# Kernel tuning notes

Hardware: AMD Instinct MI355X
Metric: run time of the kernel (lower is better)

The kernel has to match this reference:

```python
import jax, jax.numpy as jnp
import numpy as np

DIM = 512
DIM_EDGES = 64
LN_EPS = 1e-5


def setup_inputs() -> dict:
    key = jax.random.key(0)
    ks = jax.random.split(key, 4)
    b, n = 2, 768
    x = jax.random.normal(ks[0], (b, n, DIM), dtype=jnp.float32)
    # nn.Linear weights stored as [out, in], applied as x @ W.T
    W_rows = jax.random.normal(ks[1], (DIM_EDGES, DIM), dtype=jnp.float32) / np.sqrt(DIM)
    W_cols = jax.random.normal(ks[2], (DIM_EDGES, DIM), dtype=jnp.float32) / np.sqrt(DIM)
    W_edges = jax.random.normal(ks[3], (DIM_EDGES, DIM_EDGES), dtype=jnp.float32) / np.sqrt(DIM_EDGES)
    ln_gamma = jnp.ones((DIM_EDGES,), dtype=jnp.float32)
    ln_beta = jnp.zeros((DIM_EDGES,), dtype=jnp.float32)
    return {"x": x, "W_rows": W_rows, "W_cols": W_cols, "W_edges": W_edges,
            "ln_gamma": ln_gamma, "ln_beta": ln_beta}


def reference(x, W_rows, W_cols, W_edges, ln_gamma, ln_beta):
    # rows/cols: [b, n, d_e]
    rows = jnp.einsum('bnd,ed->bne', x, W_rows)
    cols = jnp.einsum('bnd,ed->bne', x, W_cols)
    # outer sum: [b, i, j, d_e]
    outer = rows[:, :, None, :] + cols[:, None, :, :]
    # edge linear (no bias): [b, i, j, d_e]
    h = jnp.einsum('bije,fe->bijf', outer, W_edges)
    # LayerNorm over last dim
    mu = jnp.mean(h, axis=-1, keepdims=True)
    var = jnp.mean(jnp.square(h - mu), axis=-1, keepdims=True)
    out = (h - mu) * jax.lax.rsqrt(var + LN_EPS) * ln_gamma + ln_beta
    return out
```

## Files before the change

### kernel.cpp

```cpp
#include <hip/hip_runtime.h>

#define B 2
#define N 768
#define DIM 512
#define DE 64
#define LN_EPS 1e-5f

#define OFF_RC   0
#define OFF_CC   (B*N*DE)
#define OFF_SSR  (2*B*N*DE)
#define OFF_SSC  (2*B*N*DE + B*N)

__global__ __launch_bounds__(256) void ee_precompute(
    const float* __restrict__ x, const float* __restrict__ Wr,
    const float* __restrict__ Wc, const float* __restrict__ We,
    float* __restrict__ Rc, float* __restrict__ Cc,
    float* __restrict__ ssqR, float* __restrict__ ssqC)
{
    __shared__ float xs[DIM];
    __shared__ float rc[2 * DE];

    const int tok = blockIdx.x;
    const int tid = threadIdx.x;
    const int lane = tid & 63;
    const int wave = tid >> 6;

    const float* xp = x + (size_t)tok * DIM;
    xs[tid]       = xp[tid];
    xs[tid + 256] = xp[tid + 256];
    __syncthreads();

    const float4 b0 = *(const float4*)(xs + lane * 8);
    const float4 b1 = *(const float4*)(xs + lane * 8 + 4);
    for (int m = 0; m < 32; ++m) {
        const int o = wave * 32 + m;
        const float* W = (o < DE) ? (Wr + (size_t)o * DIM)
                                  : (Wc + (size_t)(o - DE) * DIM);
        const float4 a0 = *(const float4*)(W + lane * 8);
        const float4 a1 = *(const float4*)(W + lane * 8 + 4);
        float p = a0.x*b0.x + a0.y*b0.y + a0.z*b0.z + a0.w*b0.w
                + a1.x*b1.x + a1.y*b1.y + a1.z*b1.z + a1.w*b1.w;
        #pragma unroll
        for (int s = 1; s < 64; s <<= 1) p += __shfl_xor(p, s);
        if (lane == 0) rc[o] = p;
    }
    __syncthreads();

    if (tid < 128) {
        const int f = lane;
        const float* W = We + (size_t)f * DE;
        const float* rcp = (wave == 0) ? rc : (rc + DE);
        float acc = 0.f;
        #pragma unroll
        for (int e4 = 0; e4 < DE / 4; ++e4) {
            const float4 w4 = *(const float4*)(W + e4 * 4);
            const float4 r4 = *(const float4*)(rcp + e4 * 4);
            acc += w4.x*r4.x + w4.y*r4.y + w4.z*r4.z + w4.w*r4.w;
        }
        float mu = acc;
        #pragma unroll
        for (int s = 1; s < 64; s <<= 1) mu += __shfl_xor(mu, s);
        mu *= (1.f / DE);
        const float c = acc - mu;
        float sq = c * c;
        #pragma unroll
        for (int s = 1; s < 64; s <<= 1) sq += __shfl_xor(sq, s);
        float* dst = ((wave == 0) ? Rc : Cc) + (size_t)tok * DE;
        dst[f] = c;
        if (lane == 0) ((wave == 0) ? ssqR : ssqC)[tok] = sq;
    }
}

__global__ __launch_bounds__(256) void ee_outer_ln(
    const float* __restrict__ Rc, const float* __restrict__ Cc,
    const float* __restrict__ ssqRp, const float* __restrict__ ssqCp,
    const float* __restrict__ gamma, const float* __restrict__ beta,
    float* __restrict__ out)
{
    const int bi = blockIdx.x;
    const int tid = threadIdx.x;
    const int lane = tid & 63;
    const int wave = tid >> 6;
    const int jsub = lane >> 4;
    const int fb = (lane & 15) * 4;

    const int b = bi / N;
    const float* Ccb   = Cc + (size_t)b * N * DE;
    const float* ssqCb = ssqCp + (size_t)b * N;
    float* outb = out + (size_t)bi * N * DE;

    const float ssqR = ssqRp[bi];
    const float4 r  = *(const float4*)(Rc + (size_t)bi * DE + fb);
    const float4 g  = *(const float4*)(gamma + fb);
    const float4 be = *(const float4*)(beta + fb);

    for (int t = 0; t < N / 16; ++t) {
        const int j = t * 16 + wave * 4 + jsub;
        const float4 c = *(const float4*)(Ccb + (size_t)j * DE + fb);
        const float ssqC = ssqCb[j];

        float p = r.x*c.x + r.y*c.y + r.z*c.z + r.w*c.w;
        p += __shfl_xor(p, 1);
        p += __shfl_xor(p, 2);
        p += __shfl_xor(p, 4);
        p += __shfl_xor(p, 8);

        const float var = (ssqR + ssqC + 2.f * p) * (1.f / DE);
        const float s = rsqrtf(var + LN_EPS);

        float4 o;
        o.x = (r.x + c.x) * (s * g.x) + be.x;
        o.y = (r.y + c.y) * (s * g.y) + be.y;
        o.z = (r.z + c.z) * (s * g.z) + be.z;
        o.w = (r.w + c.w) * (s * g.w) + be.w;
        *(float4*)(outb + (size_t)j * DE + fb) = o;
    }
}

extern "C" void kernel_launch(void* const* d_in, const int* in_sizes, int n_in,
                              void* d_out, int out_size, void* d_ws, size_t ws_size,
                              hipStream_t stream) {
    const float* x     = (const float*)d_in[0];
    const float* Wr    = (const float*)d_in[1];
    const float* Wc    = (const float*)d_in[2];
    const float* We    = (const float*)d_in[3];
    const float* gamma = (const float*)d_in[4];
    const float* beta  = (const float*)d_in[5];
    float* out = (float*)d_out;
    float* ws  = (float*)d_ws;

    float* Rc   = ws + OFF_RC;
    float* Cc   = ws + OFF_CC;
    float* ssqR = ws + OFF_SSR;
    float* ssqC = ws + OFF_SSC;

    ee_precompute<<<B * N, 256, 0, stream>>>(x, Wr, Wc, We, Rc, Cc, ssqR, ssqC);
    ee_outer_ln<<<B * N, 256, 0, stream>>>(Rc, Cc, ssqR, ssqC, gamma, beta, out);
}
```

Baseline: 343.5 us.

## Precompute per-column LN scales in LDS and use nontemporal output stores

The outer-LN kernel now runs a first pass in which each thread computes the full 64-wide dot product between the row vector (staged in LDS) and one column vector, then stores the rsqrt scale for all 768 columns in shared memory. This removes the per-iteration cross-lane shuffle reduction from the main store loop. The main loop is unrolled by four, and its 256MB output write uses nontemporal stores to avoid polluting the cache. The trade-off is a second read of the Cc matrix per block and a block-wide barrier. The strided per-thread row reads in the first pass may also be uncoalesced.

New measurement: 357.6 us. 1.04x slower.

```diff
diff --git a/kernel.cpp b/kernel.cpp
--- a/kernel.cpp
+++ b/kernel.cpp
@@ -5,6 +5,8 @@
 #define DIM 512
 #define DE 64
 #define LN_EPS 1e-5f
+
+typedef float f32x4 __attribute__((ext_vector_type(4)));
 
 #define OFF_RC   0
 #define OFF_CC   (B*N*DE)
@@ -77,6 +79,9 @@
     const float* __restrict__ gamma, const float* __restrict__ beta,
     float* __restrict__ out)
 {
+    __shared__ float rs[DE];
+    __shared__ float sj[N];
+
     const int bi = blockIdx.x;
     const int tid = threadIdx.x;
     const int lane = tid & 63;
@@ -89,31 +94,39 @@
     const float* ssqCb = ssqCp + (size_t)b * N;
     float* outb = out + (size_t)bi * N * DE;
 
+    if (tid < DE) rs[tid] = Rc[(size_t)bi * DE + tid];
+    __syncthreads();
+
     const float ssqR = ssqRp[bi];
-    const float4 r  = *(const float4*)(Rc + (size_t)bi * DE + fb);
-    const float4 g  = *(const float4*)(gamma + fb);
-    const float4 be = *(const float4*)(beta + fb);
 
+    #pragma unroll
+    for (int jt = 0; jt < N / 256; ++jt) {
+        const int j0 = jt * 256 + tid;
+        const float* cj = Ccb + (size_t)j0 * DE;
+        f32x4 a = (f32x4)(0.f);
+        #pragma unroll
+        for (int e = 0; e < DE / 4; ++e) {
+            const f32x4 w = *(const f32x4*)(rs + e * 4);
+            const f32x4 c = *(const f32x4*)(cj + e * 4);
+            a += w * c;
+        }
+        const float p = a.x + a.y + a.z + a.w;
+        const float var = (ssqR + ssqCb[j0] + 2.f * p) * (1.f / DE);
+        sj[j0] = rsqrtf(var + LN_EPS);
+    }
+    __syncthreads();
+
+    const f32x4 r  = *(const f32x4*)(rs + fb);
+    const f32x4 g  = *(const f32x4*)(gamma + fb);
+    const f32x4 be = *(const f32x4*)(beta + fb);
+
+    #pragma unroll 4
     for (int t = 0; t < N / 16; ++t) {
         const int j = t * 16 + wave * 4 + jsub;
-        const float4 c = *(const float4*)(Ccb + (size_t)j * DE + fb);
-        const float ssqC = ssqCb[j];
-
-        float p = r.x*c.x + r.y*c.y + r.z*c.z + r.w*c.w;
-        p += __shfl_xor(p, 1);
-        p += __shfl_xor(p, 2);
-        p += __shfl_xor(p, 4);
-        p += __shfl_xor(p, 8);
-
-        const float var = (ssqR + ssqC + 2.f * p) * (1.f / DE);
-        const float s = rsqrtf(var + LN_EPS);
-
-        float4 o;
-        o.x = (r.x + c.x) * (s * g.x) + be.x;
-        o.y = (r.y + c.y) * (s * g.y) + be.y;
-        o.z = (r.z + c.z) * (s * g.z) + be.z;
-        o.w = (r.w + c.w) * (s * g.w) + be.w;
-        *(float4*)(outb + (size_t)j * DE + fb) = o;
+        const f32x4 c = *(const f32x4*)(Ccb + (size_t)j * DE + fb);
+        const float s = sj[j];
+        f32x4 o = (r + c) * (s * g) + be;
+        __builtin_nontemporal_store(o, (f32x4*)(outb + (size_t)j * DE + fb));
     }
 }
 
```
